# Optimization experiments

Measured on AMD Instinct MI355X. Metric: run time of the kernel, lower is better.

## Reference

```python
import jax, jax.numpy as jnp
import numpy as np

N, E, IN_F, OUT_F, HEADS = 50000, 800000, 256, 64, 8


def setup_inputs() -> dict:
    key = jax.random.key(0)
    k1, k2, k3, k4, k5 = jax.random.split(key, 5)
    stdv = 1.0 / np.sqrt(OUT_F)
    return {
        "h": jax.random.normal(k1, (N, IN_F), dtype=jnp.float32),
        "weight": jax.random.uniform(k2, (IN_F, OUT_F), minval=-stdv, maxval=stdv, dtype=jnp.float32),
        "attention_w": jax.random.normal(k3, (1, HEADS), dtype=jnp.float32),
        "src": jax.random.randint(k4, (E,), 0, N, dtype=jnp.int32),
        "dst": jax.random.randint(k5, (E,), 0, N, dtype=jnp.int32),
    }


def reference(h, weight, attention_w, src, dst):
    n_nodes = h.shape[0]
    hp = h @ weight                              # [N, F] projected features
    hs = hp[src]                                 # [E, F] gather source feats
    hd = hp[dst]                                 # [E, F] gather dest feats
    dot = jnp.sum(hs * hd, axis=-1, keepdims=True)   # [E, 1] edge dot attention
    # original: (msg[:, F, 1] @ attention_w[1, H]).sum(H) == msg * attention_w.sum()
    msg = dot * hs * jnp.sum(attention_w)        # [E, F]
    accum = jax.ops.segment_sum(msg, dst, num_segments=n_nodes)  # [N, F]
    # DGL update_all: zero in-degree nodes keep their projected feature
    deg = jax.ops.segment_sum(jnp.ones((src.shape[0], 1), hp.dtype), dst, num_segments=n_nodes)
    return jnp.where(deg > 0, accum, hp)
```

## Files before the change

### kernel.cpp

```cpp
#include <hip/hip_runtime.h>

#define IN_F 256
#define OUT_F 64
#define NBKT_MAX 1024
#define PART_BLOCKS 128
#define CAP 3072

typedef __attribute__((ext_vector_type(8))) short short8;
typedef __attribute__((ext_vector_type(4))) float f32x4;
typedef unsigned int uint32;

#define AS_I(f) __builtin_bit_cast(int, f)
#define AS_F(i) __builtin_bit_cast(float, i)
#define DPP_ADD(v, ctrl, rmask) \
    v += AS_F(__builtin_amdgcn_update_dpp(0, AS_I(v), ctrl, rmask, 0xf, true))

__device__ __forceinline__ float half_sum_sel(float p, bool hi) {
    DPP_ADD(p, 0x111, 0xf);
    DPP_ADD(p, 0x112, 0xf);
    DPP_ADD(p, 0x114, 0xf);
    DPP_ADD(p, 0x118, 0xf);
    DPP_ADD(p, 0x142, 0xa);
    float dlo = AS_F(__builtin_amdgcn_readlane(AS_I(p), 31));
    float dhi = AS_F(__builtin_amdgcn_readlane(AS_I(p), 63));
    return hi ? dhi : dlo;
}

__device__ __forceinline__ unsigned short f2bf(float f) {
    uint32 u = __builtin_bit_cast(uint32, f);
    u += 0x7fffu + ((u >> 16) & 1u);
    return (unsigned short)(u >> 16);
}
__device__ __forceinline__ float bf2f(unsigned short s) {
    return __builtin_bit_cast(float, (uint32)s << 16);
}

__global__ __launch_bounds__(512) void gemm_part_kernel(const float* __restrict__ h,
                                                        const float* __restrict__ w,
                                                        unsigned short* __restrict__ hpb,
                                                        int N,
                                                        const int* __restrict__ src,
                                                        const int* __restrict__ dst,
                                                        int* __restrict__ tbl,
                                                        uint32* __restrict__ pairs,
                                                        int E, int NB) {
    __shared__ char smem[32768];
    __shared__ int wsum[8];
    int b = blockIdx.x, t = threadIdx.x;

    if (b < PART_BLOCKS) {
        int* lcnt = (int*)smem;
        int lane = t & 63, wid = t >> 6;
        int chunk = (E + PART_BLOCKS - 1) / PART_BLOCKS;
        int s0 = b * chunk, s1 = min(E, s0 + chunk);

        for (int i = t; i < NB; i += 512) lcnt[i] = 0;
        __syncthreads();
        for (int e = s0 + t; e < s1; e += 512)
            atomicAdd(&lcnt[dst[e] >> 6], 1);
        __syncthreads();

        int i0 = t * 2;
        int x0 = (i0     < NB) ? lcnt[i0]     : 0;
        int x1 = (i0 + 1 < NB) ? lcnt[i0 + 1] : 0;
        int s  = x0 + x1;
        int xs = s;
#pragma unroll
        for (int off = 1; off < 64; off <<= 1) {
            int y = __shfl_up(xs, off, 64);
            if (lane >= off) xs += y;
        }
        if (lane == 63) wsum[wid] = xs;
        __syncthreads();
        int basew = 0;
        for (int k = 0; k < wid; ++k) basew += wsum[k];
        int toff = basew + xs - s;

        int* trow = tbl + (size_t)b * (NB + 1);
        if (i0     < NB) { trow[i0]     = s0 + toff;      lcnt[i0]     = toff;      }
        if (i0 + 1 < NB) { trow[i0 + 1] = s0 + toff + x0; lcnt[i0 + 1] = toff + x0; }
        if (t == 0) trow[NB] = s1;
        __syncthreads();

        for (int e = s0 + t; e < s1; e += 512) {
            int d  = dst[e];
            int bk = d >> 6;
            int idx = atomicAdd(&lcnt[bk], 1);
            pairs[s0 + idx] = (uint32)src[e] | ((uint32)(d & 63) << 26);
        }
        return;
    }

    int gb = b - PART_BLOCKS;
    short8* wfrag = (short8*)smem;
    for (int slot = t; slot < 2048; slot += 512) {
        int kb = slot >> 6, n = slot & 63;
        short8 v;
#pragma unroll
        for (int jj = 0; jj < 8; ++jj)
            v[jj] = (short)f2bf(w[(size_t)(kb * 8 + jj) * OUT_F + n]);
        wfrag[slot] = v;
    }
    __syncthreads();

    int wave = t >> 6, lane = t & 63;
    int n16  = lane & 15, quad = lane >> 4;
    int base = gb * 128 + wave * 16;
    int arow_i = base + n16; if (arow_i >= N) arow_i = N - 1;
    const float* arow = h + (size_t)arow_i * IN_F;

    f32x4 acc[4];
#pragma unroll
    for (int ct = 0; ct < 4; ++ct) acc[ct] = (f32x4){0.f, 0.f, 0.f, 0.f};

#pragma unroll
    for (int ks = 0; ks < 8; ++ks) {
        int k0 = ks * 32;
        float4 a0 = *(const float4*)(arow + k0 + quad * 8);
        float4 a1 = *(const float4*)(arow + k0 + quad * 8 + 4);
        short8 af;
        af[0] = (short)f2bf(a0.x); af[1] = (short)f2bf(a0.y);
        af[2] = (short)f2bf(a0.z); af[3] = (short)f2bf(a0.w);
        af[4] = (short)f2bf(a1.x); af[5] = (short)f2bf(a1.y);
        af[6] = (short)f2bf(a1.z); af[7] = (short)f2bf(a1.w);
        int kb = ks * 4 + quad;
#pragma unroll
        for (int ct = 0; ct < 4; ++ct) {
            short8 bf = wfrag[kb * 64 + ct * 16 + n16];
            acc[ct] = __builtin_amdgcn_mfma_f32_16x16x32_bf16(af, bf, acc[ct], 0, 0, 0);
        }
    }

#pragma unroll
    for (int ct = 0; ct < 4; ++ct) {
#pragma unroll
        for (int r = 0; r < 4; ++r) {
            int ro = base + quad * 4 + r;
            if (ro < N) hpb[(size_t)ro * OUT_F + ct * 16 + n16] = f2bf(acc[ct][r]);
        }
    }
}

#define GATH(S) (*(const uint32*)(hpb + (size_t)(S) * OUT_F + half * 2))
#define PROC(Q) { float a0 = bf2f((unsigned short)((Q) & 0xffff));            \
                  float a1 = bf2f((unsigned short)((Q) >> 16));               \
                  float dd = half_sum_sel(fmaf(a1, hd1, a0 * hd0), hi);       \
                  acc0 = fmaf(dd, a0, acc0); acc1 = fmaf(dd, a1, acc1); }

__global__ __launch_bounds__(512) void accum_kernel(const unsigned short* __restrict__ hpb,
                                                    const uint32* __restrict__ pairs,
                                                    const int* __restrict__ tbl,
                                                    const float* __restrict__ attw,
                                                    float* __restrict__ out, int N, int NB) {
    __shared__ uint32 sraw[CAP];
    __shared__ int slds[CAP];
    __shared__ int segb[PART_BLOCKS], slen[PART_BLOCKS], psum[PART_BLOCKS + 1];
    __shared__ int bin[64], excl[65], cur[64];

    int b = blockIdx.x, t = threadIdx.x;
    int wid = t >> 6, lane = t & 63;
    int half = lane & 31;
    bool hi  = lane >= 32;
    int node0 = b * 64;

    if (t < PART_BLOCKS) {
        const int* trow = tbl + (size_t)t * (NB + 1);
        int b0 = trow[b];
        segb[t] = b0;
        slen[t] = trow[b + 1] - b0;
    }
    __syncthreads();
    if (wid == 0) {
        int l0 = slen[lane * 2], l1 = slen[lane * 2 + 1];
        int s = l0 + l1, xs = s;
#pragma unroll
        for (int off = 1; off < 64; off <<= 1) {
            int y = __shfl_up(xs, off, 64);
            if (lane >= off) xs += y;
        }
        int ex = xs - s;
        psum[lane * 2]     = ex;
        psum[lane * 2 + 1] = ex + l0;
        if (lane == 63) psum[PART_BLOCKS] = xs;
    }
    __syncthreads();
    int nE = psum[PART_BLOCKS];

    float c = 0.f;
#pragma unroll
    for (int i = 0; i < 8; ++i) c += attw[i];

    if (nE <= CAP) {
        for (int i = t; i < nE; i += 512) {
            int lo = 0, hh = PART_BLOCKS - 1;
#pragma unroll
            for (int it = 0; it < 7; ++it) {
                int mid = (lo + hh + 1) >> 1;
                if (psum[mid] <= i) lo = mid; else hh = mid - 1;
            }
            sraw[i] = pairs[segb[lo] + (i - psum[lo])];
        }
        if (t < 64) bin[t] = 0;
        __syncthreads();
        for (int i = t; i < nE; i += 512)
            atomicAdd(&bin[sraw[i] >> 26], 1);
        __syncthreads();
        if (t < 64) {
            int v = bin[t], x = v;
#pragma unroll
            for (int off = 1; off < 64; off <<= 1) {
                int y = __shfl_up(x, off, 64);
                if (t >= off) x += y;
            }
            excl[t] = x - v;
            cur[t]  = x - v;
            if (t == 63) excl[64] = x;
        }
        __syncthreads();
        for (int i = t; i < nE; i += 512) {
            uint32 p = sraw[i];
            int pos = atomicAdd(&cur[(int)(p >> 26)], 1);
            slds[pos] = (int)(p & 0x3FFFFFFu);
        }
        __syncthreads();

#pragma unroll 1
        for (int k = 0; k < 8; ++k) {
            int n    = wid + 8 * k;
            int node = node0 + n;
            if (node >= N) continue;

            int jb = excl[n], je = excl[n + 1];

            uint32 hd2 = *(const uint32*)(hpb + (size_t)node * OUT_F + half * 2);
            float hd0 = bf2f((unsigned short)(hd2 & 0xffff));
            float hd1 = bf2f((unsigned short)(hd2 >> 16));

            float acc0 = 0.f, acc1 = 0.f;
            int j = jb;
            int sel = hi ? 1 : 0;

            for (; j + 16 <= je; j += 16) {
                int i0 = slds[j + 0  + sel], i1 = slds[j + 2  + sel];
                int i2 = slds[j + 4  + sel], i3 = slds[j + 6  + sel];
                int i4 = slds[j + 8  + sel], i5 = slds[j + 10 + sel];
                int i6 = slds[j + 12 + sel], i7 = slds[j + 14 + sel];
                uint32 q0 = GATH(i0), q1 = GATH(i1), q2 = GATH(i2), q3 = GATH(i3);
                uint32 q4 = GATH(i4), q5 = GATH(i5), q6 = GATH(i6), q7 = GATH(i7);
                PROC(q0) PROC(q1) PROC(q2) PROC(q3)
                PROC(q4) PROC(q5) PROC(q6) PROC(q7)
            }
            for (; j + 8 <= je; j += 8) {
                int i0 = slds[j + 0 + sel], i1 = slds[j + 2 + sel];
                int i2 = slds[j + 4 + sel], i3 = slds[j + 6 + sel];
                uint32 q0 = GATH(i0), q1 = GATH(i1), q2 = GATH(i2), q3 = GATH(i3);
                PROC(q0) PROC(q1) PROC(q2) PROC(q3)
            }
            for (; j + 2 <= je; j += 2) {
                int i0 = slds[j + sel];
                uint32 q0 = GATH(i0);
                PROC(q0)
            }
            if (j < je) {
                int i0 = slds[j];
                uint32 q0 = GATH(i0);
                float a0 = bf2f((unsigned short)(q0 & 0xffff));
                float a1 = bf2f((unsigned short)(q0 >> 16));
                float dd = half_sum_sel(fmaf(a1, hd1, a0 * hd0), false);
                if (!hi) {
                    acc0 = fmaf(dd, a0, acc0);
                    acc1 = fmaf(dd, a1, acc1);
                }
            }

            acc0 += __shfl_xor(acc0, 32, 64);
            acc1 += __shfl_xor(acc1, 32, 64);

            if (!hi) {
                float r0, r1;
                if (je > jb) { r0 = acc0 * c; r1 = acc1 * c; }
                else         { r0 = hd0;      r1 = hd1;      }
                *(float2*)(out + (size_t)node * OUT_F + half * 2) = make_float2(r0, r1);
            }
        }
    } else {
#pragma unroll 1
        for (int k = 0; k < 8; ++k) {
            int n    = wid + 8 * k;
            int node = node0 + n;
            if (node >= N) continue;

            uint32 hd2 = *(const uint32*)(hpb + (size_t)node * OUT_F + half * 2);
            float hd0 = bf2f((unsigned short)(hd2 & 0xffff));
            float hd1 = bf2f((unsigned short)(hd2 >> 16));

            float acc0 = 0.f, acc1 = 0.f;
            int deg = 0;
            for (int p = 0; p < PART_BLOCKS; ++p) {
                int bb = segb[p], ee = bb + slen[p];
                for (int i = bb; i < ee; ++i) {
                    uint32 pr = pairs[i];
                    if ((int)(pr >> 26) == n) {
                        ++deg;
                        uint32 q0 = GATH((int)(pr & 0x3FFFFFFu));
                        float a0 = bf2f((unsigned short)(q0 & 0xffff));
                        float a1 = bf2f((unsigned short)(q0 >> 16));
                        float dd = half_sum_sel(fmaf(a1, hd1, a0 * hd0), false);
                        if (!hi) {
                            acc0 = fmaf(dd, a0, acc0);
                            acc1 = fmaf(dd, a1, acc1);
                        }
                    }
                }
            }
            acc0 += __shfl_xor(acc0, 32, 64);
            acc1 += __shfl_xor(acc1, 32, 64);
            if (!hi) {
                float r0, r1;
                if (deg > 0) { r0 = acc0 * c; r1 = acc1 * c; }
                else         { r0 = hd0;      r1 = hd1;      }
                *(float2*)(out + (size_t)node * OUT_F + half * 2) = make_float2(r0, r1);
            }
        }
    }
}

extern "C" void kernel_launch(void* const* d_in, const int* in_sizes, int n_in,
                              void* d_out, int out_size, void* d_ws, size_t ws_size,
                              hipStream_t stream) {
    const float* h    = (const float*)d_in[0];
    const float* w    = (const float*)d_in[1];
    const float* attw = (const float*)d_in[2];
    const int*   src  = (const int*)d_in[3];
    const int*   dst  = (const int*)d_in[4];

    int N = in_sizes[0] / IN_F;
    int E = in_sizes[3];
    int NB = (N + 63) >> 6;
    int ngemm = (N + 127) / 128;

    float* out = (float*)d_out;

    char* p = (char*)d_ws;
    unsigned short* hpb = (unsigned short*)p;  p += (size_t)N * OUT_F * sizeof(unsigned short);
    int* tbl      = (int*)p;                   p += (size_t)PART_BLOCKS * (NBKT_MAX + 1) * sizeof(int);
    uint32* pairs = (uint32*)p;

    gemm_part_kernel<<<PART_BLOCKS + ngemm, 512, 0, stream>>>(h, w, hpb, N,
                                                              src, dst, tbl, pairs, E, NB);

    accum_kernel<<<NB, 512, 0, stream>>>(hpb, pairs, tbl, attw, out, N, NB);
}
```

Baseline: 139.6 us.

## Stage dst in LDS, double GEMM rows per wave, fuse binning, prefetch dest features

In the partition blocks, each chunk's dst indices are now kept in shared memory so the second pass reads them from LDS instead of global memory. In the GEMM, each wave computes 32 rows instead of 16, reusing each weight fragment across two MFMAs, and the grid is halved. In the accumulate kernel, bucket counting is folded into the pair-loading loop, which removes a barrier and a second pass. The destination-node feature for the next iteration is also prefetched. The trade-offs are higher register pressure and fewer GEMM blocks available to overlap with partitioning.

```diff
diff --git a/kernel.cpp b/kernel.cpp
--- a/kernel.cpp
+++ b/kernel.cpp
@@ -5,6 +5,7 @@
 #define NBKT_MAX 1024
 #define PART_BLOCKS 128
 #define CAP 3072
+#define DSTBUF_CAP 7168
 
 typedef __attribute__((ext_vector_type(8))) short short8;
 typedef __attribute__((ext_vector_type(4))) float f32x4;
@@ -49,15 +50,25 @@
     int b = blockIdx.x, t = threadIdx.x;
 
     if (b < PART_BLOCKS) {
-        int* lcnt = (int*)smem;
+        int* lcnt   = (int*)smem;
+        int* dstbuf = (int*)smem + NBKT_MAX;
         int lane = t & 63, wid = t >> 6;
         int chunk = (E + PART_BLOCKS - 1) / PART_BLOCKS;
         int s0 = b * chunk, s1 = min(E, s0 + chunk);
+        bool stageDst = (s1 - s0) <= DSTBUF_CAP;
 
         for (int i = t; i < NB; i += 512) lcnt[i] = 0;
         __syncthreads();
-        for (int e = s0 + t; e < s1; e += 512)
-            atomicAdd(&lcnt[dst[e] >> 6], 1);
+        if (stageDst) {
+            for (int e = s0 + t; e < s1; e += 512) {
+                int d = dst[e];
+                dstbuf[e - s0] = d;
+                atomicAdd(&lcnt[d >> 6], 1);
+            }
+        } else {
+            for (int e = s0 + t; e < s1; e += 512)
+                atomicAdd(&lcnt[dst[e] >> 6], 1);
+        }
         __syncthreads();
 
         int i0 = t * 2;
@@ -83,7 +94,7 @@
         __syncthreads();
 
         for (int e = s0 + t; e < s1; e += 512) {
-            int d  = dst[e];
+            int d  = stageDst ? dstbuf[e - s0] : dst[e];
             int bk = d >> 6;
             int idx = atomicAdd(&lcnt[bk], 1);
             pairs[s0 + idx] = (uint32)src[e] | ((uint32)(d & 63) << 26);
@@ -105,38 +116,52 @@
 
     int wave = t >> 6, lane = t & 63;
     int n16  = lane & 15, quad = lane >> 4;
-    int base = gb * 128 + wave * 16;
-    int arow_i = base + n16; if (arow_i >= N) arow_i = N - 1;
-    const float* arow = h + (size_t)arow_i * IN_F;
-
-    f32x4 acc[4];
-#pragma unroll
-    for (int ct = 0; ct < 4; ++ct) acc[ct] = (f32x4){0.f, 0.f, 0.f, 0.f};
+    int base = gb * 256 + wave * 32;
+    int ra = base + n16;      if (ra >= N) ra = N - 1;
+    int rb = base + 16 + n16; if (rb >= N) rb = N - 1;
+    const float* arow0 = h + (size_t)ra * IN_F;
+    const float* arow1 = h + (size_t)rb * IN_F;
+
+    f32x4 acc[2][4];
+#pragma unroll
+    for (int m = 0; m < 2; ++m)
+#pragma unroll
+        for (int ct = 0; ct < 4; ++ct) acc[m][ct] = (f32x4){0.f, 0.f, 0.f, 0.f};
 
 #pragma unroll
     for (int ks = 0; ks < 8; ++ks) {
         int k0 = ks * 32;
-        float4 a0 = *(const float4*)(arow + k0 + quad * 8);
-        float4 a1 = *(const float4*)(arow + k0 + quad * 8 + 4);
-        short8 af;
+        float4 a0 = *(const float4*)(arow0 + k0 + quad * 8);
+        float4 a1 = *(const float4*)(arow0 + k0 + quad * 8 + 4);
+        float4 b0 = *(const float4*)(arow1 + k0 + quad * 8);
+        float4 b1 = *(const float4*)(arow1 + k0 + quad * 8 + 4);
+        short8 af, ag;
         af[0] = (short)f2bf(a0.x); af[1] = (short)f2bf(a0.y);
         af[2] = (short)f2bf(a0.z); af[3] = (short)f2bf(a0.w);
         af[4] = (short)f2bf(a1.x); af[5] = (short)f2bf(a1.y);
         af[6] = (short)f2bf(a1.z); af[7] = (short)f2bf(a1.w);
+        ag[0] = (short)f2bf(b0.x); ag[1] = (short)f2bf(b0.y);
+        ag[2] = (short)f2bf(b0.z); ag[3] = (short)f2bf(b0.w);
+        ag[4] = (short)f2bf(b1.x); ag[5] = (short)f2bf(b1.y);
+        ag[6] = (short)f2bf(b1.z); ag[7] = (short)f2bf(b1.w);
         int kb = ks * 4 + quad;
 #pragma unroll
         for (int ct = 0; ct < 4; ++ct) {
-            short8 bf = wfrag[kb * 64 + ct * 16 + n16];
-            acc[ct] = __builtin_amdgcn_mfma_f32_16x16x32_bf16(af, bf, acc[ct], 0, 0, 0);
-        }
-    }
-
-#pragma unroll
-    for (int ct = 0; ct < 4; ++ct) {
-#pragma unroll
-        for (int r = 0; r < 4; ++r) {
-            int ro = base + quad * 4 + r;
-            if (ro < N) hpb[(size_t)ro * OUT_F + ct * 16 + n16] = f2bf(acc[ct][r]);
+            short8 bw = wfrag[kb * 64 + ct * 16 + n16];
+            acc[0][ct] = __builtin_amdgcn_mfma_f32_16x16x32_bf16(af, bw, acc[0][ct], 0, 0, 0);
+            acc[1][ct] = __builtin_amdgcn_mfma_f32_16x16x32_bf16(ag, bw, acc[1][ct], 0, 0, 0);
+        }
+    }
+
+#pragma unroll
+    for (int m = 0; m < 2; ++m) {
+#pragma unroll
+        for (int ct = 0; ct < 4; ++ct) {
+#pragma unroll
+            for (int r = 0; r < 4; ++r) {
+                int ro = base + m * 16 + quad * 4 + r;
+                if (ro < N) hpb[(size_t)ro * OUT_F + ct * 16 + n16] = f2bf(acc[m][ct][r]);
+            }
         }
     }
 }
@@ -183,6 +208,7 @@
         psum[lane * 2 + 1] = ex + l0;
         if (lane == 63) psum[PART_BLOCKS] = xs;
     }
+    if (wid == 1) bin[lane] = 0;
     __syncthreads();
     int nE = psum[PART_BLOCKS];
 
@@ -198,12 +224,10 @@
                 int mid = (lo + hh + 1) >> 1;
                 if (psum[mid] <= i) lo = mid; else hh = mid - 1;
             }
-            sraw[i] = pairs[segb[lo] + (i - psum[lo])];
-        }
-        if (t < 64) bin[t] = 0;
-        __syncthreads();
-        for (int i = t; i < nE; i += 512)
-            atomicAdd(&bin[sraw[i] >> 26], 1);
+            uint32 p = pairs[segb[lo] + (i - psum[lo])];
+            sraw[i] = p;
+            atomicAdd(&bin[p >> 26], 1);
+        }
         __syncthreads();
         if (t < 64) {
             int v = bin[t], x = v;
@@ -224,64 +248,71 @@
         }
         __syncthreads();
 
+        int a0i = min(node0 + wid, N - 1);
+        uint32 hd2 = *(const uint32*)(hpb + (size_t)a0i * OUT_F + half * 2);
 #pragma unroll 1
         for (int k = 0; k < 8; ++k) {
-            int n    = wid + 8 * k;
-            int node = node0 + n;
-            if (node >= N) continue;
-
-            int jb = excl[n], je = excl[n + 1];
-
-            uint32 hd2 = *(const uint32*)(hpb + (size_t)node * OUT_F + half * 2);
-            float hd0 = bf2f((unsigned short)(hd2 & 0xffff));
-            float hd1 = bf2f((unsigned short)(hd2 >> 16));
-
-            float acc0 = 0.f, acc1 = 0.f;
-            int j = jb;
-            int sel = hi ? 1 : 0;
-
-            for (; j + 16 <= je; j += 16) {
-                int i0 = slds[j + 0  + sel], i1 = slds[j + 2  + sel];
-                int i2 = slds[j + 4  + sel], i3 = slds[j + 6  + sel];
-                int i4 = slds[j + 8  + sel], i5 = slds[j + 10 + sel];
-                int i6 = slds[j + 12 + sel], i7 = slds[j + 14 + sel];
-                uint32 q0 = GATH(i0), q1 = GATH(i1), q2 = GATH(i2), q3 = GATH(i3);
-                uint32 q4 = GATH(i4), q5 = GATH(i5), q6 = GATH(i6), q7 = GATH(i7);
-                PROC(q0) PROC(q1) PROC(q2) PROC(q3)
-                PROC(q4) PROC(q5) PROC(q6) PROC(q7)
-            }
-            for (; j + 8 <= je; j += 8) {
-                int i0 = slds[j + 0 + sel], i1 = slds[j + 2 + sel];
-                int i2 = slds[j + 4 + sel], i3 = slds[j + 6 + sel];
-                uint32 q0 = GATH(i0), q1 = GATH(i1), q2 = GATH(i2), q3 = GATH(i3);
-                PROC(q0) PROC(q1) PROC(q2) PROC(q3)
-            }
-            for (; j + 2 <= je; j += 2) {
-                int i0 = slds[j + sel];
-                uint32 q0 = GATH(i0);
-                PROC(q0)
-            }
-            if (j < je) {
-                int i0 = slds[j];
-                uint32 q0 = GATH(i0);
-                float a0 = bf2f((unsigned short)(q0 & 0xffff));
-                float a1 = bf2f((unsigned short)(q0 >> 16));
-                float dd = half_sum_sel(fmaf(a1, hd1, a0 * hd0), false);
+            int node = node0 + wid + 8 * k;
+            uint32 hd2n = 0;
+            if (k < 7) {
+                int an = min(node + 8, N - 1);
+                hd2n = *(const uint32*)(hpb + (size_t)an * OUT_F + half * 2);
+            }
+            if (node < N) {
+                int n  = wid + 8 * k;
+                int jb = excl[n], je = excl[n + 1];
+
+                float hd0 = bf2f((unsigned short)(hd2 & 0xffff));
+                float hd1 = bf2f((unsigned short)(hd2 >> 16));
+
+                float acc0 = 0.f, acc1 = 0.f;
+                int j = jb;
+                int sel = hi ? 1 : 0;
+
+                for (; j + 16 <= je; j += 16) {
+                    int i0 = slds[j + 0  + sel], i1 = slds[j + 2  + sel];
+                    int i2 = slds[j + 4  + sel], i3 = slds[j + 6  + sel];
+                    int i4 = slds[j + 8  + sel], i5 = slds[j + 10 + sel];
+                    int i6 = slds[j + 12 + sel], i7 = slds[j + 14 + sel];
+                    uint32 q0 = GATH(i0), q1 = GATH(i1), q2 = GATH(i2), q3 = GATH(i3);
+                    uint32 q4 = GATH(i4), q5 = GATH(i5), q6 = GATH(i6), q7 = GATH(i7);
+                    PROC(q0) PROC(q1) PROC(q2) PROC(q3)
+                    PROC(q4) PROC(q5) PROC(q6) PROC(q7)
+                }
+                for (; j + 8 <= je; j += 8) {
+                    int i0 = slds[j + 0 + sel], i1 = slds[j + 2 + sel];
+                    int i2 = slds[j + 4 + sel], i3 = slds[j + 6 + sel];
+                    uint32 q0 = GATH(i0), q1 = GATH(i1), q2 = GATH(i2), q3 = GATH(i3);
+                    PROC(q0) PROC(q1) PROC(q2) PROC(q3)
+                }
+                for (; j + 2 <= je; j += 2) {
+                    int i0 = slds[j + sel];
+                    uint32 q0 = GATH(i0);
+                    PROC(q0)
+                }
+                if (j < je) {
+                    int i0 = slds[j];
+                    uint32 q0 = GATH(i0);
+                    float a0 = bf2f((unsigned short)(q0 & 0xffff));
+                    float a1 = bf2f((unsigned short)(q0 >> 16));
+                    float dd = half_sum_sel(fmaf(a1, hd1, a0 * hd0), false);
+                    if (!hi) {
+                        acc0 = fmaf(dd, a0, acc0);
+                        acc1 = fmaf(dd, a1, acc1);
+                    }
+                }
+
+                acc0 += __shfl_xor(acc0, 32, 64);
+                acc1 += __shfl_xor(acc1, 32, 64);
+
                 if (!hi) {
-                    acc0 = fmaf(dd, a0, acc0);
-                    acc1 = fmaf(dd, a1, acc1);
-                }
-            }
-
-            acc0 += __shfl_xor(acc0, 32, 64);
-            acc1 += __shfl_xor(acc1, 32, 64);
-
-            if (!hi) {
-                float r0, r1;
-                if (je > jb) { r0 = acc0 * c; r1 = acc1 * c; }
-                else         { r0 = hd0;      r1 = hd1;      }
-                *(float2*)(out + (size_t)node * OUT_F + half * 2) = make_float2(r0, r1);
-            }
+                    float r0, r1;
+                    if (je > jb) { r0 = acc0 * c; r1 = acc1 * c; }
+                    else         { r0 = hd0;      r1 = hd1;      }
+                    *(float2*)(out + (size_t)node * OUT_F + half * 2) = make_float2(r0, r1);
+                }
+            }
+            hd2 = hd2n;
         }
     } else {
 #pragma unroll 1
@@ -337,7 +368,7 @@
     int N = in_sizes[0] / IN_F;
     int E = in_sizes[3];
     int NB = (N + 63) >> 6;
-    int ngemm = (N + 127) / 128;
+    int ngemm = (N + 255) / 256;
 
     float* out = (float*)d_out;
 
```

Result: no change. 139.5 us (-0.1%).
